# Performance work log

Measured on AMD Instinct MI355X. Metric: run time of the kernel, lower is better.

Reference implementation:

```python
import jax, jax.numpy as jnp
import numpy as np

NUM_RAYS = 262144   # 512x512 image
NUM_BINS = 128      # coarse samples per ray
NUM_SAMPLES = 128   # fine samples per ray (init arg)
EPS = 1e-05


def setup_inputs() -> dict:
    key = jax.random.key(0)
    k1, k2 = jax.random.split(key)
    weights = jax.random.uniform(k1, (NUM_RAYS, NUM_BINS), dtype=jnp.float32)
    u = jax.random.uniform(k2, (NUM_RAYS, NUM_SAMPLES), dtype=jnp.float32)
    return {"weights": weights, "u": u, "stratified": 1}


def reference(weights, u, stratified):
    # --- pdf normalization (visible torch code) ---
    num_bins = weights.shape[-1]
    num_samples = u.shape[-1]
    weights_sum = jnp.sum(weights, axis=-1, keepdims=True)
    padding = jax.nn.relu(EPS - weights_sum)
    weights = weights + padding / num_bins
    weights_sum = weights_sum + padding
    pdf = weights / weights_sum                                   # [R, B]

    # --- CDF ---
    cdf = jnp.cumsum(pdf, axis=-1)
    cdf = jnp.concatenate([jnp.zeros_like(cdf[..., :1]), cdf], axis=-1)  # [R, B+1]

    # --- stratified / deterministic uniforms in [0,1) ---
    strata = jnp.arange(num_samples, dtype=weights.dtype)
    if stratified:
        us = (strata + u) / num_samples                           # [R, S]
    else:
        us = jnp.broadcast_to((strata + 0.5) / num_samples, u.shape)

    # --- inverse-CDF: searchsorted + gather + lerp ---
    inds = jax.vmap(lambda c, uu: jnp.searchsorted(c, uu, side='right'))(cdf, us)
    below = jnp.clip(inds - 1, 0, num_bins)                       # [R, S]
    above = jnp.clip(inds, 0, num_bins)
    cdf_b = jnp.take_along_axis(cdf, below, axis=-1)
    cdf_a = jnp.take_along_axis(cdf, above, axis=-1)
    bins = jnp.linspace(0.0, 1.0, num_bins + 1, dtype=weights.dtype)  # normalized bin edges
    bins_b = bins[below]
    bins_a = bins[above]
    denom = cdf_a - cdf_b
    denom = jnp.where(denom < 1e-5, jnp.ones_like(denom), denom)
    t = (us - cdf_b) / denom
    samples = bins_b + t * (bins_a - bins_b)                      # [R, S]
    return samples
```

## Files before the change

### kernel.cpp

```cpp
#include <hip/hip_runtime.h>


typedef float f32x2 __attribute__((ext_vector_type(2)));

constexpr int NUM_BINS    = 128;
constexpr int NUM_SAMPLES = 128;
constexpr float EPS_PAD   = 1e-5f;
constexpr float INV_S     = 1.0f / 128.0f;
constexpr int RPB         = 4;

template <int CTRL, int ROW_MASK>
__device__ __forceinline__ float dpp_add(float x) {
    int s = __builtin_amdgcn_update_dpp(0, __float_as_int(x), CTRL, ROW_MASK, 0xf, true);
    return x + __int_as_float(s);
}

__global__ __launch_bounds__(256) void ray_sampler_kernel(
    const float* __restrict__ W,
    const float* __restrict__ U,
    const int*   __restrict__ stratp,
    float*       __restrict__ out)
{
    const int wave = threadIdx.x >> 6;
    const int lane = threadIdx.x & 63;
    const int ray  = blockIdx.x * RPB + wave;

    __shared__ float cdf_s[RPB][NUM_BINS + 4];

    const f32x2 w2 = *reinterpret_cast<const f32x2*>(W + (size_t)ray * NUM_BINS + 2 * lane);
    const float pair = w2.x + w2.y;

    float incl = pair;
    incl = dpp_add<0x111, 0xf>(incl);
    incl = dpp_add<0x112, 0xf>(incl);
    incl = dpp_add<0x114, 0xf>(incl);
    incl = dpp_add<0x118, 0xf>(incl);
    incl = dpp_add<0x142, 0xa>(incl);
    incl = dpp_add<0x143, 0xc>(incl);
    const float total = __shfl(incl, 63, 64);

    const float padding = fmaxf(EPS_PAD - total, 0.0f);
    const float ppb     = padding * INV_S;
    const float inv     = __builtin_amdgcn_rcpf(total + padding);

    const float pre = incl - pair;
    float* cw = cdf_s[wave];
    cw[2 * lane + 1] = (pre + w2.x + (float)(2 * lane + 1) * ppb) * inv;
    cw[2 * lane + 2] = (incl        + (float)(2 * lane + 2) * ppb) * inv;

    asm volatile("s_waitcnt lgkmcnt(0)" ::: "memory");

    const int strat = *stratp;
    const f32x2 u2 = *reinterpret_cast<const f32x2*>(U + (size_t)ray * NUM_SAMPLES + 2 * lane);
    const float uu0 = strat ? u2.x : 0.5f;
    const float uu1 = strat ? u2.y : 0.5f;
    const float us0 = ((float)(2 * lane)     + uu0) * INV_S;
    const float us1 = ((float)(2 * lane + 1) + uu1) * INV_S;

    const float* cdf = cw;
    int a0 = 0, a1 = 0;
    float cb0 = 0.0f, cb1 = 0.0f;
    #pragma unroll
    for (int step = 64; step; step >>= 1) {
        const float c0 = cdf[a0 + step];
        const float c1 = cdf[a1 + step];
        if (c0 <= us0) { a0 += step; cb0 = c0; }
        if (c1 <= us1) { a1 += step; cb1 = c1; }
    }
    const float ca0 = cdf[a0 + 1];
    const float ca1 = cdf[a1 + 1];

    float d0 = ca0 - cb0;  d0 = (d0 < 1e-5f) ? 1.0f : d0;
    float d1 = ca1 - cb1;  d1 = (d1 < 1e-5f) ? 1.0f : d1;
    const float t0 = (us0 - cb0) * __builtin_amdgcn_rcpf(d0);
    const float t1 = (us1 - cb1) * __builtin_amdgcn_rcpf(d1);

    f32x2 o;
    o.x = ((float)a0 + t0) * INV_S;
    o.y = ((float)a1 + t1) * INV_S;
    __builtin_nontemporal_store(o,
        reinterpret_cast<f32x2*>(out + (size_t)ray * NUM_SAMPLES + 2 * lane));
}

extern "C" void kernel_launch(void* const* d_in, const int* in_sizes, int n_in,
                              void* d_out, int out_size, void* d_ws, size_t ws_size,
                              hipStream_t stream) {
    const float* W     = (const float*)d_in[0];
    const float* U     = (const float*)d_in[1];
    const int*   strat = (const int*)d_in[2];
    float*       out   = (float*)d_out;

    const int num_rays = in_sizes[0] / NUM_BINS;
    const int blocks   = num_rays / RPB;
    hipLaunchKernelGGL(ray_sampler_kernel, dim3(blocks), dim3(256), 0, stream,
                       W, U, strat, out);
}
```

Measured before the change: 69.80 us.

## Map each ray to a half-wave with 128-bit loads and four samples per lane

Each 32-lane half-wave now handles one ray, so each lane does four bins and four samples. Global loads and stores widen from 64-bit to 128-bit, and the U load moves up to issue alongside the weights load. The DPP scan drops its final cross-row step because it only spans 32 lanes. The shared CDF no longer stores the leading zero and the search indices shift by one to match. Each lane now runs four independent binary searches, which adds register pressure but gives more LDS-latency overlap per lane.

```diff
diff --git a/kernel.cpp b/kernel.cpp
--- a/kernel.cpp
+++ b/kernel.cpp
@@ -2,12 +2,13 @@
 
 
 typedef float f32x2 __attribute__((ext_vector_type(2)));
+typedef float f32x4 __attribute__((ext_vector_type(4)));
 
 constexpr int NUM_BINS    = 128;
-constexpr int NUM_SAMPLES = 128;
 constexpr float EPS_PAD   = 1e-5f;
 constexpr float INV_S     = 1.0f / 128.0f;
-constexpr int RPB         = 4;
+constexpr int WPB         = 4;
+constexpr int RPB         = 8;
 
 template <int CTRL, int ROW_MASK>
 __device__ __forceinline__ float dpp_add(float x) {
@@ -23,63 +24,85 @@
 {
     const int wave = threadIdx.x >> 6;
     const int lane = threadIdx.x & 63;
-    const int ray  = blockIdx.x * RPB + wave;
+    const int h    = lane >> 5;
+    const int sl   = lane & 31;
+    const int ray  = blockIdx.x * RPB + wave * 2 + h;
 
-    __shared__ float cdf_s[RPB][NUM_BINS + 4];
+    __shared__ float cdf_s[RPB][132];
+    float* cw = cdf_s[wave * 2 + h];
 
-    const f32x2 w2 = *reinterpret_cast<const f32x2*>(W + (size_t)ray * NUM_BINS + 2 * lane);
-    const float pair = w2.x + w2.y;
+    const size_t rb = (size_t)ray * NUM_BINS;
+    const int b = 4 * sl;
 
-    float incl = pair;
+    const f32x4 w4 = *reinterpret_cast<const f32x4*>(W + rb + b);
+    const f32x4 u4 = *reinterpret_cast<const f32x4*>(U + rb + b);
+
+    const float s1 = w4.x;
+    const float s2 = s1 + w4.y;
+    const float s3 = s2 + w4.z;
+    const float quad = s3 + w4.w;
+
+    float incl = quad;
     incl = dpp_add<0x111, 0xf>(incl);
     incl = dpp_add<0x112, 0xf>(incl);
     incl = dpp_add<0x114, 0xf>(incl);
     incl = dpp_add<0x118, 0xf>(incl);
     incl = dpp_add<0x142, 0xa>(incl);
-    incl = dpp_add<0x143, 0xc>(incl);
-    const float total = __shfl(incl, 63, 64);
 
-    const float padding = fmaxf(EPS_PAD - total, 0.0f);
+    const float tot = __shfl(incl, 31 | (lane & 32), 64);
+    const float padding = fmaxf(EPS_PAD - tot, 0.0f);
     const float ppb     = padding * INV_S;
-    const float inv     = __builtin_amdgcn_rcpf(total + padding);
+    const float inv     = __builtin_amdgcn_rcpf(tot + padding);
+    const float pre     = incl - quad;
 
-    const float pre = incl - pair;
-    float* cw = cdf_s[wave];
-    cw[2 * lane + 1] = (pre + w2.x + (float)(2 * lane + 1) * ppb) * inv;
-    cw[2 * lane + 2] = (incl        + (float)(2 * lane + 2) * ppb) * inv;
+    f32x4 st;
+    st.x = (pre + s1   + (float)(b + 1) * ppb) * inv;
+    st.y = (pre + s2   + (float)(b + 2) * ppb) * inv;
+    st.z = (pre + s3   + (float)(b + 3) * ppb) * inv;
+    st.w = (pre + quad + (float)(b + 4) * ppb) * inv;
+    *reinterpret_cast<f32x4*>(cw + b) = st;
 
     asm volatile("s_waitcnt lgkmcnt(0)" ::: "memory");
 
     const int strat = *stratp;
-    const f32x2 u2 = *reinterpret_cast<const f32x2*>(U + (size_t)ray * NUM_SAMPLES + 2 * lane);
-    const float uu0 = strat ? u2.x : 0.5f;
-    const float uu1 = strat ? u2.y : 0.5f;
-    const float us0 = ((float)(2 * lane)     + uu0) * INV_S;
-    const float us1 = ((float)(2 * lane + 1) + uu1) * INV_S;
+    const float uu0 = strat ? u4.x : 0.5f;
+    const float uu1 = strat ? u4.y : 0.5f;
+    const float uu2 = strat ? u4.z : 0.5f;
+    const float uu3 = strat ? u4.w : 0.5f;
+    const float us0 = ((float)(b + 0) + uu0) * INV_S;
+    const float us1 = ((float)(b + 1) + uu1) * INV_S;
+    const float us2 = ((float)(b + 2) + uu2) * INV_S;
+    const float us3 = ((float)(b + 3) + uu3) * INV_S;
 
-    const float* cdf = cw;
-    int a0 = 0, a1 = 0;
-    float cb0 = 0.0f, cb1 = 0.0f;
+    int a0 = 0, a1 = 0, a2 = 0, a3 = 0;
+    float cb0 = 0.0f, cb1 = 0.0f, cb2 = 0.0f, cb3 = 0.0f;
     #pragma unroll
     for (int step = 64; step; step >>= 1) {
-        const float c0 = cdf[a0 + step];
-        const float c1 = cdf[a1 + step];
+        const float c0 = cw[a0 + step - 1];
+        const float c1 = cw[a1 + step - 1];
+        const float c2 = cw[a2 + step - 1];
+        const float c3 = cw[a3 + step - 1];
         if (c0 <= us0) { a0 += step; cb0 = c0; }
         if (c1 <= us1) { a1 += step; cb1 = c1; }
+        if (c2 <= us2) { a2 += step; cb2 = c2; }
+        if (c3 <= us3) { a3 += step; cb3 = c3; }
     }
-    const float ca0 = cdf[a0 + 1];
-    const float ca1 = cdf[a1 + 1];
+    const float ca0 = cw[a0];
+    const float ca1 = cw[a1];
+    const float ca2 = cw[a2];
+    const float ca3 = cw[a3];
 
     float d0 = ca0 - cb0;  d0 = (d0 < 1e-5f) ? 1.0f : d0;
     float d1 = ca1 - cb1;  d1 = (d1 < 1e-5f) ? 1.0f : d1;
-    const float t0 = (us0 - cb0) * __builtin_amdgcn_rcpf(d0);
-    const float t1 = (us1 - cb1) * __builtin_amdgcn_rcpf(d1);
+    float d2 = ca2 - cb2;  d2 = (d2 < 1e-5f) ? 1.0f : d2;
+    float d3 = ca3 - cb3;  d3 = (d3 < 1e-5f) ? 1.0f : d3;
 
-    f32x2 o;
-    o.x = ((float)a0 + t0) * INV_S;
-    o.y = ((float)a1 + t1) * INV_S;
-    __builtin_nontemporal_store(o,
-        reinterpret_cast<f32x2*>(out + (size_t)ray * NUM_SAMPLES + 2 * lane));
+    f32x4 o;
+    o.x = ((float)a0 + (us0 - cb0) * __builtin_amdgcn_rcpf(d0)) * INV_S;
+    o.y = ((float)a1 + (us1 - cb1) * __builtin_amdgcn_rcpf(d1)) * INV_S;
+    o.z = ((float)a2 + (us2 - cb2) * __builtin_amdgcn_rcpf(d2)) * INV_S;
+    o.w = ((float)a3 + (us3 - cb3) * __builtin_amdgcn_rcpf(d3)) * INV_S;
+    __builtin_nontemporal_store(o, reinterpret_cast<f32x4*>(out + rb + b));
 }
 
 extern "C" void kernel_launch(void* const* d_in, const int* in_sizes, int n_in,
```

Result: faster. 62.20 us (-10.9%).

## Map each ray to a 16-lane group with 8 samples per lane

Applied to the files above, without the earlier changes.

Each wave now handles four rays: every 16-lane group scans one ray using float4 loads of the weights and a 16-lane DPP scan, and each lane binary-searches 8 samples instead of 2. The shared CDF array drops the explicit leading zero, so search indices and bracket handling are adjusted. The aim is more independent LDS lookups per lane to hide latency and a shorter cross-lane scan, at the cost of more registers and strided scalar loads and stores for U and the output.

```diff
diff --git a/kernel.cpp b/kernel.cpp
--- a/kernel.cpp
+++ b/kernel.cpp
@@ -1,13 +1,13 @@
 #include <hip/hip_runtime.h>
 
 
-typedef float f32x2 __attribute__((ext_vector_type(2)));
+typedef float f32x4 __attribute__((ext_vector_type(4)));
 
-constexpr int NUM_BINS    = 128;
-constexpr int NUM_SAMPLES = 128;
-constexpr float EPS_PAD   = 1e-5f;
-constexpr float INV_S     = 1.0f / 128.0f;
-constexpr int RPB         = 4;
+constexpr int NUM_BINS = 128;
+constexpr float EPS_PAD = 1e-5f;
+constexpr float INV_S   = 1.0f / 128.0f;
+constexpr int RPB       = 16;
+constexpr int STRIDE    = 136;
 
 template <int CTRL, int ROW_MASK>
 __device__ __forceinline__ float dpp_add(float x) {
@@ -23,63 +23,88 @@
 {
     const int wave = threadIdx.x >> 6;
     const int lane = threadIdx.x & 63;
-    const int ray  = blockIdx.x * RPB + wave;
+    const int g    = lane >> 4;
+    const int sl   = lane & 15;
+    const int ray  = blockIdx.x * RPB + wave * 4 + g;
 
-    __shared__ float cdf_s[RPB][NUM_BINS + 4];
+    __shared__ float cdf_s[RPB][STRIDE];
+    float* cw = cdf_s[wave * 4 + g];
 
-    const f32x2 w2 = *reinterpret_cast<const f32x2*>(W + (size_t)ray * NUM_BINS + 2 * lane);
-    const float pair = w2.x + w2.y;
+    const size_t rb = (size_t)ray * NUM_BINS;
+    const int strat = *stratp;
 
-    float incl = pair;
-    incl = dpp_add<0x111, 0xf>(incl);
-    incl = dpp_add<0x112, 0xf>(incl);
-    incl = dpp_add<0x114, 0xf>(incl);
-    incl = dpp_add<0x118, 0xf>(incl);
-    incl = dpp_add<0x142, 0xa>(incl);
-    incl = dpp_add<0x143, 0xc>(incl);
-    const float total = __shfl(incl, 63, 64);
+    const f32x4 qA = *reinterpret_cast<const f32x4*>(W + rb + 4 * sl);
+    const f32x4 qB = *reinterpret_cast<const f32x4*>(W + rb + 64 + 4 * sl);
+    float ur[8];
+    #pragma unroll
+    for (int c = 0; c < 8; ++c) ur[c] = U[rb + 16 * c + sl];
 
-    const float padding = fmaxf(EPS_PAD - total, 0.0f);
+    const float a1 = qA.x, a2 = a1 + qA.y, a3 = a2 + qA.z, a4 = a3 + qA.w;
+    const float b1 = qB.x, b2 = b1 + qB.y, b3 = b2 + qB.z, b4 = b3 + qB.w;
+
+    float iA = a4, iB = b4;
+    iA = dpp_add<0x111, 0xf>(iA);  iB = dpp_add<0x111, 0xf>(iB);
+    iA = dpp_add<0x112, 0xf>(iA);  iB = dpp_add<0x112, 0xf>(iB);
+    iA = dpp_add<0x114, 0xf>(iA);  iB = dpp_add<0x114, 0xf>(iB);
+    iA = dpp_add<0x118, 0xf>(iA);  iB = dpp_add<0x118, 0xf>(iB);
+
+    const float totA = __shfl(iA, lane | 15, 64);
+    const float totB = __shfl(iB, lane | 15, 64);
+    const float tot  = totA + totB;
+
+    const float padding = fmaxf(EPS_PAD - tot, 0.0f);
     const float ppb     = padding * INV_S;
-    const float inv     = __builtin_amdgcn_rcpf(total + padding);
+    const float inv     = __builtin_amdgcn_rcpf(tot + padding);
+    const float preA    = iA - a4;
+    const float preB    = iB - b4;
 
-    const float pre = incl - pair;
-    float* cw = cdf_s[wave];
-    cw[2 * lane + 1] = (pre + w2.x + (float)(2 * lane + 1) * ppb) * inv;
-    cw[2 * lane + 2] = (incl        + (float)(2 * lane + 2) * ppb) * inv;
+    const int bA = 4 * sl, bB = 64 + 4 * sl;
+    f32x4 stA, stB;
+    stA.x = (preA + a1 + (float)(bA + 1) * ppb) * inv;
+    stA.y = (preA + a2 + (float)(bA + 2) * ppb) * inv;
+    stA.z = (preA + a3 + (float)(bA + 3) * ppb) * inv;
+    stA.w = (preA + a4 + (float)(bA + 4) * ppb) * inv;
+    stB.x = (totA + preB + b1 + (float)(bB + 1) * ppb) * inv;
+    stB.y = (totA + preB + b2 + (float)(bB + 2) * ppb) * inv;
+    stB.z = (totA + preB + b3 + (float)(bB + 3) * ppb) * inv;
+    stB.w = (totA + preB + b4 + (float)(bB + 4) * ppb) * inv;
+    *reinterpret_cast<f32x4*>(cw + bA) = stA;
+    *reinterpret_cast<f32x4*>(cw + bB) = stB;
 
     asm volatile("s_waitcnt lgkmcnt(0)" ::: "memory");
 
-    const int strat = *stratp;
-    const f32x2 u2 = *reinterpret_cast<const f32x2*>(U + (size_t)ray * NUM_SAMPLES + 2 * lane);
-    const float uu0 = strat ? u2.x : 0.5f;
-    const float uu1 = strat ? u2.y : 0.5f;
-    const float us0 = ((float)(2 * lane)     + uu0) * INV_S;
-    const float us1 = ((float)(2 * lane + 1) + uu1) * INV_S;
+    float us[8];
+    #pragma unroll
+    for (int c = 0; c < 8; ++c) {
+        const float uu = strat ? ur[c] : 0.5f;
+        us[c] = ((float)(16 * c + sl) + uu) * INV_S;
+    }
 
-    const float* cdf = cw;
-    int a0 = 0, a1 = 0;
-    float cb0 = 0.0f, cb1 = 0.0f;
+    int av[8];
+    #pragma unroll
+    for (int c = 0; c < 8; ++c) av[c] = 0;
     #pragma unroll
     for (int step = 64; step; step >>= 1) {
-        const float c0 = cdf[a0 + step];
-        const float c1 = cdf[a1 + step];
-        if (c0 <= us0) { a0 += step; cb0 = c0; }
-        if (c1 <= us1) { a1 += step; cb1 = c1; }
+        #pragma unroll
+        for (int c = 0; c < 8; ++c) {
+            const float v = cw[av[c] + (step - 1)];
+            if (v <= us[c]) av[c] += step;
+        }
     }
-    const float ca0 = cdf[a0 + 1];
-    const float ca1 = cdf[a1 + 1];
 
-    float d0 = ca0 - cb0;  d0 = (d0 < 1e-5f) ? 1.0f : d0;
-    float d1 = ca1 - cb1;  d1 = (d1 < 1e-5f) ? 1.0f : d1;
-    const float t0 = (us0 - cb0) * __builtin_amdgcn_rcpf(d0);
-    const float t1 = (us1 - cb1) * __builtin_amdgcn_rcpf(d1);
-
-    f32x2 o;
-    o.x = ((float)a0 + t0) * INV_S;
-    o.y = ((float)a1 + t1) * INV_S;
-    __builtin_nontemporal_store(o,
-        reinterpret_cast<f32x2*>(out + (size_t)ray * NUM_SAMPLES + 2 * lane));
+    #pragma unroll
+    for (int c = 0; c < 8; ++c) {
+        const int a = av[c];
+        const int m = a ? a - 1 : 0;
+        const float lo = cw[m], hi = cw[m + 1];
+        const float cb = a ? lo : 0.0f;
+        const float ca = a ? hi : lo;
+        float d = ca - cb;
+        d = (d < 1e-5f) ? 1.0f : d;
+        const float t = (us[c] - cb) * __builtin_amdgcn_rcpf(d);
+        const float o = ((float)a + t) * INV_S;
+        __builtin_nontemporal_store(o, out + rb + 16 * c + sl);
+    }
 }
 
 extern "C" void kernel_launch(void* const* d_in, const int* in_sizes, int n_in,
```

Measured after the change: 64.97 us. -6.9%, faster.
